# Kernel tuning notes

Measured on AMD Instinct MI355X. Metric: run time of the kernel, lower is better.

Reference implementation:

```python
import jax, jax.numpy as jnp
import numpy as np

DIM = 768
N_HEADS = 12
HEAD_DIM = DIM // N_HEADS
MLP_DIM = 3072
DEPTH = 12
B, N = 16, 512


def setup_inputs() -> dict:
    key = jax.random.key(0)
    ks = jax.random.split(key, 12)
    s = 0.02
    return {
        "x": jax.random.normal(ks[0], (B, N, DIM), dtype=jnp.float32),
        "ln_w": jnp.ones((DIM,), jnp.float32),
        "ln_b": jnp.zeros((DIM,), jnp.float32),
        "wq": jax.random.normal(ks[1], (DIM, DIM), jnp.float32) * s,
        "bq": jnp.zeros((DIM,), jnp.float32),
        "wk": jax.random.normal(ks[2], (DIM, DIM), jnp.float32) * s,
        "bk": jnp.zeros((DIM,), jnp.float32),
        "wv": jax.random.normal(ks[3], (DIM, DIM), jnp.float32) * s,
        "bv": jnp.zeros((DIM,), jnp.float32),
        "w1": jax.random.normal(ks[4], (DIM, MLP_DIM), jnp.float32) * s,
        "b1": jnp.zeros((MLP_DIM,), jnp.float32),
        "w2": jax.random.normal(ks[5], (MLP_DIM, DIM), jnp.float32) * s,
        "b2": jnp.zeros((DIM,), jnp.float32),
    }


def _layernorm(x, w, b):
    mu = jnp.mean(x, axis=-1, keepdims=True)
    var = jnp.var(x, axis=-1, keepdims=True)
    return (x - mu) * jax.lax.rsqrt(var + 1e-5) * w + b


def _mha(x, wq, bq, wk, bk, wv, bv):
    # x: [b, n, dim]; weights stored as [in, out]
    def heads(t):
        return t.reshape(B, N, N_HEADS, HEAD_DIM).transpose(0, 2, 1, 3)  # b h n d
    q = heads(x @ wq + bq)
    k = heads(x @ wk + bk)
    v = heads(x @ wv + bv)
    scores = jnp.einsum('bhqd,bhkd->bhqk', q, k) / np.sqrt(HEAD_DIM).astype(np.float32)
    attn = jax.nn.softmax(scores, axis=-1)
    o = jnp.einsum('bhqk,bhkd->bhqd', attn, v)
    return o.transpose(0, 2, 1, 3).reshape(B, N, DIM)


def reference(x, ln_w, ln_b, wq, bq, wk, bk, wv, bv, w1, b1, w2, b2):
    # Dropout is identity in eval mode. Same weights reused each depth iteration.
    for _ in range(DEPTH):
        x = _mha(_layernorm(x, ln_w, ln_b), wq, bq, wk, bk, wv, bv) + x
        h = _layernorm(x, ln_w, ln_b)
        h = jax.nn.gelu(h @ w1 + b1, approximate=False) @ w2 + b2
        x = h + x
    return x
```

## Files before the change

kernel.cpp:

```cpp
#include <hip/hip_runtime.h>

typedef __bf16 bf16x8 __attribute__((ext_vector_type(8)));
typedef float f32x4 __attribute__((ext_vector_type(4)));
typedef unsigned short ushort8_t __attribute__((ext_vector_type(8)));
typedef unsigned short ushort4_t __attribute__((ext_vector_type(4)));

#define MFMA16(a, b, c) __builtin_amdgcn_mfma_f32_16x16x32_bf16((a), (b), (c), 0, 0, 0)

#define GLOAD16(gp, lp)                                                        \
  __builtin_amdgcn_global_load_lds(                                            \
      (__attribute__((address_space(1))) void*)(gp),                           \
      (__attribute__((address_space(3))) void*)(lp), 16, 0, 0)

__device__ __forceinline__ unsigned short f2bf(float f) {
  unsigned u = __builtin_bit_cast(unsigned, f);
  return (unsigned short)((u + 0x7FFFu + ((u >> 16) & 1u)) >> 16);
}

__global__ __launch_bounds__(256) void transpose_f2b(
    const float* __restrict__ src, unsigned short* __restrict__ dst,
    int Kdim, int Ndim) {
  long i = (long)blockIdx.x * 256 + threadIdx.x;
  if (i >= (long)Kdim * Ndim) return;
  int n = (int)(i / Kdim);
  int kk = (int)(i - (long)n * Kdim);
  dst[i] = f2bf(src[(long)kk * Ndim + n]);
}

__global__ __launch_bounds__(256) void ln_kernel(
    const float* __restrict__ x, const float* __restrict__ gw,
    const float* __restrict__ gb, unsigned short* __restrict__ h) {
  const int row = blockIdx.x * 4 + (threadIdx.x >> 6);
  const int l = threadIdx.x & 63;
  const float* xr = x + (long)row * 768;
  f32x4 va[3];
#pragma unroll
  for (int i = 0; i < 3; i++) va[i] = *(const f32x4*)(xr + i * 256 + l * 4);
  float s = 0.f, ss = 0.f;
#pragma unroll
  for (int i = 0; i < 3; i++)
#pragma unroll
    for (int j = 0; j < 4; j++) {
      float t = va[i][j];
      s += t;
      ss += t * t;
    }
#pragma unroll
  for (int off = 1; off < 64; off <<= 1) {
    s += __shfl_xor(s, off, 64);
    ss += __shfl_xor(ss, off, 64);
  }
  const float mu = s * (1.f / 768.f);
  const float var = ss * (1.f / 768.f) - mu * mu;
  const float inv = rsqrtf(var + 1e-5f);
  unsigned short* hp = h + (long)row * 768;
#pragma unroll
  for (int i = 0; i < 3; i++) {
    f32x4 wv = *(const f32x4*)(gw + i * 256 + l * 4);
    f32x4 bv = *(const f32x4*)(gb + i * 256 + l * 4);
    ushort4_t o;
#pragma unroll
    for (int j = 0; j < 4; j++) o[j] = f2bf((va[i][j] - mu) * inv * wv[j] + bv[j]);
    *(ushort4_t*)(hp + i * 256 + l * 4) = o;
  }
}

__global__ __launch_bounds__(256) void transpose_v(
    const unsigned short* __restrict__ v, unsigned short* __restrict__ vt) {
  __shared__ unsigned short t[64 * 65];
  const int n0 = blockIdx.x * 64;
  const int bh = blockIdx.y;
  const int tid = threadIdx.x;
  {
    const int n = tid >> 2, d0 = (tid & 3) * 16;
    const unsigned short* s = v + ((long)bh * 512 + n0 + n) * 64 + d0;
    ushort8_t r0 = *(const ushort8_t*)s;
    ushort8_t r1 = *(const ushort8_t*)(s + 8);
#pragma unroll
    for (int j = 0; j < 8; j++) {
      t[n * 65 + d0 + j] = r0[j];
      t[n * 65 + d0 + 8 + j] = r1[j];
    }
  }
  __syncthreads();
  {
    const int d = tid >> 2, nb = (tid & 3) * 16;
    ushort8_t r0, r1;
#pragma unroll
    for (int j = 0; j < 8; j++) {
      r0[j] = t[(nb + j) * 65 + d];
      r1[j] = t[(nb + 8 + j) * 65 + d];
    }
    unsigned short* o = vt + ((long)bh * 64 + d) * 512 + n0 + nb;
    *(ushort8_t*)o = r0;
    *(ushort8_t*)(o + 8) = r1;
  }
}

enum { EPI_QKV = 0, EPI_GELU = 1, EPI_RES = 2 };

template <int EPI, int MREP>
__global__ __launch_bounds__(256) void gemm_bt(
    const unsigned short* __restrict__ A, const unsigned short* __restrict__ BT,
    int K, const float* __restrict__ bb0, const float* __restrict__ bb1,
    const float* __restrict__ bb2, unsigned short* __restrict__ o0,
    unsigned short* __restrict__ o1, unsigned short* __restrict__ o2,
    float* oF) {
  constexpr int BM = MREP * 32;
  constexpr int ABUF = BM * 32;
  __shared__ unsigned short As[2][ABUF];
  __shared__ unsigned short Bs[2][128 * 32];
  const int tid = threadIdx.x;
  const int w = tid >> 6, l = tid & 63;
  const int lr = l & 15, lg = l >> 4;
  const int wr = w >> 1, wc = w & 1;

  const int nx = gridDim.x;
  const int nwg = nx * gridDim.y;
  int wg = blockIdx.y * nx + blockIdx.x;
  {
    const int qq = nwg >> 3, rr = nwg & 7;
    const int xcd = wg & 7, idx = wg >> 3;
    wg = (xcd < rr ? xcd * (qq + 1) : rr * (qq + 1) + (xcd - rr) * qq) + idx;
  }
  const int bx = wg % nx, by = wg / nx;
  const int m0 = by * BM, n0 = bx * 128;

  const unsigned short* Ag =
      A + (long)(m0 + w * (BM / 4) + (l >> 2)) * K + (l & 3) * 8;
  const unsigned short* Bg = BT + (long)(n0 + w * 32 + (l >> 2)) * K + (l & 3) * 8;
  unsigned short* AsW = &As[0][w * (BM / 4) * 32 + l * 8];
  unsigned short* BsW = &Bs[0][w * 1024 + l * 8];

  auto stage = [&](int buf, int kt) {
    const unsigned short* ag = Ag + kt * 32;
    const unsigned short* bg = Bg + kt * 32;
    unsigned short* aw = AsW + buf * ABUF;
    unsigned short* bw = BsW + buf * 4096;
#pragma unroll
    for (int i = 0; i < BM / 64; i++) GLOAD16(ag + i * 16 * K, aw + i * 512);
    GLOAD16(bg, bw);
    GLOAD16(bg + 16 * K, bw + 512);
  };

  f32x4 acc[MREP][4] = {};
  const int nk = K >> 5;
  stage(0, 0);
  __syncthreads();
  for (int kt = 0; kt < nk; ++kt) {
    const int cur = kt & 1;
    if (kt + 1 < nk) stage(cur ^ 1, kt + 1);
    const unsigned short* Ab = &As[cur][0];
    const unsigned short* Bb = &Bs[cur][0];
    bf16x8 a[MREP], b[4];
#pragma unroll
    for (int i = 0; i < MREP; i++)
      a[i] = *(const bf16x8*)(Ab + (wr * MREP * 16 + i * 16 + lr) * 32 + lg * 8);
#pragma unroll
    for (int j = 0; j < 4; j++)
      b[j] = *(const bf16x8*)(Bb + (wc * 64 + j * 16 + lr) * 32 + lg * 8);
#pragma unroll
    for (int i = 0; i < MREP; i++)
#pragma unroll
      for (int j = 0; j < 4; j++) acc[i][j] = MFMA16(a[i], b[j], acc[i][j]);
    __syncthreads();
  }

  if (EPI == EPI_QKV) {
    const int whichq = n0 / 768;
    const int cc0 = n0 - whichq * 768;
    const float* bias = whichq == 0 ? bb0 : whichq == 1 ? bb1 : bb2;
    unsigned short* dst = whichq == 0 ? o0 : whichq == 1 ? o1 : o2;
#pragma unroll
    for (int i = 0; i < MREP; i++) {
      const int r = m0 + wr * MREP * 16 + i * 16 + lg * 4;
#pragma unroll
      for (int j = 0; j < 4; j++) {
        const int ccol = cc0 + wc * 64 + j * 16 + lr;
        const int hd = ccol >> 6, d = ccol & 63;
        const float bv = bias[ccol];
#pragma unroll
        for (int q = 0; q < 4; q++) {
          const int row = r + q;
          const int bidx = row >> 9, n = row & 511;
          const long addr = ((long)(bidx * 12 + hd) * 512 + n) * 64 + d;
          dst[addr] = f2bf(acc[i][j][q] + bv);
        }
      }
    }
  } else if (EPI == EPI_GELU) {
#pragma unroll
    for (int i = 0; i < MREP; i++) {
      const int r = m0 + wr * MREP * 16 + i * 16 + lg * 4;
#pragma unroll
      for (int j = 0; j < 4; j++) {
        const int c = n0 + wc * 64 + j * 16 + lr;
        const float bv = bb0[c];
#pragma unroll
        for (int q = 0; q < 4; q++) {
          float v = acc[i][j][q] + bv;
          const float u = v * (0.7978845608f + 0.0356774081f * v * v);
          const float g = v / (1.0f + __expf(-2.0f * u));
          o0[(long)(r + q) * 3072 + c] = f2bf(g);
        }
      }
    }
  } else {
#pragma unroll
    for (int i = 0; i < MREP; i++) {
      const int r = m0 + wr * MREP * 16 + i * 16 + lg * 4;
#pragma unroll
      for (int j = 0; j < 4; j++) {
        const int c = n0 + wc * 64 + j * 16 + lr;
        const float bv = bb0[c];
#pragma unroll
        for (int q = 0; q < 4; q++) {
          const long addr = (long)(r + q) * 768 + c;
          oF[addr] = acc[i][j][q] + bv + oF[addr];
        }
      }
    }
  }
}

__global__ __launch_bounds__(256) void attn_kernel(
    const unsigned short* __restrict__ qg, const unsigned short* __restrict__ kg,
    const unsigned short* __restrict__ vtg, float* __restrict__ x) {
  __shared__ unsigned short Qs[128 * 64];
  __shared__ unsigned short Ks[2][64 * 64];
  __shared__ unsigned short Vt[2][64 * 64];
  __shared__ unsigned short Ps[4][32 * 64];
  const int qt = blockIdx.x, h = blockIdx.y, b = blockIdx.z;
  const int bh = b * 12 + h;
  const int tid = threadIdx.x, w = tid >> 6, l = tid & 63;
  const int lr = l & 15, lg = l >> 4;

  const unsigned short* qrow =
      qg + ((long)bh * 512 + qt * 128 + w * 32 + (l >> 3)) * 64 + (l & 7) * 8;
  unsigned short* QsW = &Qs[w * 2048 + l * 8];
#pragma unroll
  for (int cc = 0; cc < 4; cc++) GLOAD16(qrow + cc * 8 * 64, QsW + cc * 512);

  const unsigned short* krow =
      kg + ((long)bh * 512 + w * 16 + (l >> 3)) * 64 + (l & 7) * 8;
  const unsigned short* vrow =
      vtg + ((long)bh * 64 + w * 16 + (l >> 3)) * 512 + (l & 7) * 8;
  unsigned short* KsW = &Ks[0][w * 1024 + l * 8];
  unsigned short* VtW = &Vt[0][w * 1024 + l * 8];
  unsigned short* Pw = &Ps[w][0];

  auto stageKV = [&](int buf, int kt) {
#pragma unroll
    for (int cc = 0; cc < 2; cc++) {
      GLOAD16(krow + (kt * 64 + cc * 8) * 64, KsW + buf * 4096 + cc * 512);
      GLOAD16(vrow + cc * 8 * 512 + kt * 64, VtW + buf * 4096 + cc * 512);
    }
  };
  stageKV(0, 0);
  __syncthreads();

  bf16x8 qa[2][2];
#pragma unroll
  for (int mi = 0; mi < 2; mi++)
#pragma unroll
    for (int ds = 0; ds < 2; ds++) {
      qa[mi][ds] =
          *(const bf16x8*)(Qs + (w * 32 + mi * 16 + lr) * 64 + ds * 32 + lg * 8);
#pragma unroll
      for (int e = 0; e < 8; e++)
        qa[mi][ds][e] = (__bf16)(0.125f * (float)qa[mi][ds][e]);
    }

  float lsum[8] = {};
  f32x4 o[2][4] = {};

  for (int kt = 0; kt < 8; ++kt) {
    const int cur = kt & 1;
    if (kt < 7) stageKV(cur ^ 1, kt + 1);

    f32x4 s[2][4] = {};
#pragma unroll
    for (int ds = 0; ds < 2; ++ds) {
      bf16x8 kb[4];
#pragma unroll
      for (int nj = 0; nj < 4; nj++)
        kb[nj] = *(const bf16x8*)(&Ks[cur][0] + (nj * 16 + lr) * 64 + ds * 32 + lg * 8);
#pragma unroll
      for (int mi = 0; mi < 2; mi++)
#pragma unroll
        for (int nj = 0; nj < 4; nj++) s[mi][nj] = MFMA16(qa[mi][ds], kb[nj], s[mi][nj]);
    }

#pragma unroll
    for (int mi = 0; mi < 2; mi++)
#pragma unroll
      for (int nj = 0; nj < 4; nj++)
#pragma unroll
        for (int q = 0; q < 4; q++) {
          const float p = __expf(s[mi][nj][q]);
          lsum[mi * 4 + q] += p;
          Pw[(mi * 16 + lg * 4 + q) * 64 + nj * 16 + lr] = f2bf(p);
        }

#pragma unroll
    for (int ks = 0; ks < 2; ++ks) {
      bf16x8 pa[2], vb[4];
#pragma unroll
      for (int mi = 0; mi < 2; mi++)
        pa[mi] = *(const bf16x8*)(Pw + (mi * 16 + lr) * 64 + ks * 32 + lg * 8);
#pragma unroll
      for (int dj = 0; dj < 4; dj++)
        vb[dj] = *(const bf16x8*)(&Vt[cur][0] + (dj * 16 + lr) * 64 + ks * 32 + lg * 8);
#pragma unroll
      for (int mi = 0; mi < 2; mi++)
#pragma unroll
        for (int dj = 0; dj < 4; dj++) o[mi][dj] = MFMA16(pa[mi], vb[dj], o[mi][dj]);
    }
    __syncthreads();
  }

#pragma unroll
  for (int i = 0; i < 8; i++) {
#pragma unroll
    for (int off = 1; off < 16; off <<= 1) lsum[i] += __shfl_xor(lsum[i], off, 64);
  }

#pragma unroll
  for (int mi = 0; mi < 2; mi++) {
#pragma unroll
    for (int q = 0; q < 4; q++) {
      const int n = qt * 128 + w * 32 + mi * 16 + lg * 4 + q;
      const float inv = 1.0f / lsum[mi * 4 + q];
      const long base = ((long)(b * 512 + n)) * 768 + h * 64;
#pragma unroll
      for (int dj = 0; dj < 4; dj++) {
        const long a = base + dj * 16 + lr;
        x[a] = x[a] + o[mi][dj][q] * inv;
      }
    }
  }
}

extern "C" void kernel_launch(void* const* d_in, const int* in_sizes, int n_in,
                              void* d_out, int out_size, void* d_ws,
                              size_t ws_size, hipStream_t stream) {
  const float* x_in = (const float*)d_in[0];
  const float* ln_w = (const float*)d_in[1];
  const float* ln_b = (const float*)d_in[2];
  const float* wq = (const float*)d_in[3];
  const float* bq = (const float*)d_in[4];
  const float* wk = (const float*)d_in[5];
  const float* bk = (const float*)d_in[6];
  const float* wv = (const float*)d_in[7];
  const float* bv = (const float*)d_in[8];
  const float* w1 = (const float*)d_in[9];
  const float* b1 = (const float*)d_in[10];
  const float* w2 = (const float*)d_in[11];
  const float* b2 = (const float*)d_in[12];

  char* p = (char*)d_ws;
  float* xw = (float*)p;            p += 8192L * 768 * 4;
  unsigned short* hbuf = (unsigned short*)p;  p += 8192L * 768 * 2;
  unsigned short* wqkvT = (unsigned short*)p; p += 2304L * 768 * 2;
  unsigned short* w1T = (unsigned short*)p;   p += 3072L * 768 * 2;
  unsigned short* w2T = (unsigned short*)p;   p += 768L * 3072 * 2;
  unsigned short* qb = (unsigned short*)p;
  unsigned short* kb = qb + 6291456L;
  unsigned short* vb = kb + 6291456L;
  unsigned short* vt = vb + 6291456L;
  unsigned short* gbuf = qb;

  hipMemcpyAsync(xw, x_in, 8192L * 768 * 4, hipMemcpyDeviceToDevice, stream);

  transpose_f2b<<<(768 * 768 + 255) / 256, 256, 0, stream>>>(wq, wqkvT, 768, 768);
  transpose_f2b<<<(768 * 768 + 255) / 256, 256, 0, stream>>>(wk, wqkvT + 589824L, 768, 768);
  transpose_f2b<<<(768 * 768 + 255) / 256, 256, 0, stream>>>(wv, wqkvT + 1179648L, 768, 768);
  transpose_f2b<<<(768 * 3072 + 255) / 256, 256, 0, stream>>>(w1, w1T, 768, 3072);
  transpose_f2b<<<(768 * 3072 + 255) / 256, 256, 0, stream>>>(w2, w2T, 3072, 768);

  for (int layer = 0; layer < 12; ++layer) {
    ln_kernel<<<2048, 256, 0, stream>>>(xw, ln_w, ln_b, hbuf);
    gemm_bt<EPI_QKV, 4><<<dim3(18, 64), 256, 0, stream>>>(
        hbuf, wqkvT, 768, bq, bk, bv, qb, kb, vb, nullptr);
    transpose_v<<<dim3(8, 192), 256, 0, stream>>>(vb, vt);
    attn_kernel<<<dim3(4, 12, 16), 256, 0, stream>>>(qb, kb, vt, xw);
    ln_kernel<<<2048, 256, 0, stream>>>(xw, ln_w, ln_b, hbuf);
    gemm_bt<EPI_GELU, 4><<<dim3(24, 64), 256, 0, stream>>>(
        hbuf, w1T, 768, b1, nullptr, nullptr, gbuf, nullptr, nullptr, nullptr);
    gemm_bt<EPI_RES, 2><<<dim3(6, 128), 256, 0, stream>>>(
        gbuf, w2T, 3072, b2, nullptr, nullptr, nullptr, nullptr, nullptr, xw);
  }

  hipMemcpyAsync(d_out, xw, 8192L * 768 * 4, hipMemcpyDeviceToDevice, stream);
}
```

Before: 2.856 ms.

## Store GEMM and attention LDS tiles in MFMA fragment order

Reorganizes the shared-memory layout of GEMM A/B tiles and attention Q/K/V/P tiles so that each 16x32 MFMA operand sub-tile is stored contiguously in the order lanes read it. Global-to-LDS loads now write lane-ordered 16-byte chunks, and fragment reads become a simple l*8 offset. The aim is to remove LDS bank conflicts on the 64-byte-stride fragment reads and simplify address arithmetic. In exchange, global loads now fetch 64-byte row segments per 16-row group, which may reduce coalescing per instruction, and the P write pattern changes.

```diff
diff --git a/kernel.cpp b/kernel.cpp
--- a/kernel.cpp
+++ b/kernel.cpp
@@ -107,9 +107,10 @@
     unsigned short* __restrict__ o1, unsigned short* __restrict__ o2,
     float* oF) {
   constexpr int BM = MREP * 32;
-  constexpr int ABUF = BM * 32;
+  constexpr int ASUB = 2 * MREP;
+  constexpr int ABUF = ASUB * 512;
   __shared__ unsigned short As[2][ABUF];
-  __shared__ unsigned short Bs[2][128 * 32];
+  __shared__ unsigned short Bs[2][8 * 512];
   const int tid = threadIdx.x;
   const int w = tid >> 6, l = tid & 63;
   const int lr = l & 15, lg = l >> 4;
@@ -126,21 +127,21 @@
   const int bx = wg % nx, by = wg / nx;
   const int m0 = by * BM, n0 = bx * 128;
 
-  const unsigned short* Ag =
-      A + (long)(m0 + w * (BM / 4) + (l >> 2)) * K + (l & 3) * 8;
-  const unsigned short* Bg = BT + (long)(n0 + w * 32 + (l >> 2)) * K + (l & 3) * 8;
-  unsigned short* AsW = &As[0][w * (BM / 4) * 32 + l * 8];
-  unsigned short* BsW = &Bs[0][w * 1024 + l * 8];
+  const unsigned short* Agl = A + (long)(m0 + lr) * K + lg * 8;
+  const unsigned short* Bgl = BT + (long)(n0 + lr) * K + lg * 8;
 
   auto stage = [&](int buf, int kt) {
-    const unsigned short* ag = Ag + kt * 32;
-    const unsigned short* bg = Bg + kt * 32;
-    unsigned short* aw = AsW + buf * ABUF;
-    unsigned short* bw = BsW + buf * 4096;
-#pragma unroll
-    for (int i = 0; i < BM / 64; i++) GLOAD16(ag + i * 16 * K, aw + i * 512);
-    GLOAD16(bg, bw);
-    GLOAD16(bg + 16 * K, bw + 512);
+    const int kk = kt * 32;
+#pragma unroll
+    for (int t = 0; t < ASUB / 4; t++) {
+      const int s = w + t * 4;
+      GLOAD16(Agl + (long)(s * 16) * K + kk, &As[buf][s * 512 + l * 8]);
+    }
+#pragma unroll
+    for (int t = 0; t < 2; t++) {
+      const int s = w + t * 4;
+      GLOAD16(Bgl + (long)(s * 16) * K + kk, &Bs[buf][s * 512 + l * 8]);
+    }
   };
 
   f32x4 acc[MREP][4] = {};
@@ -150,15 +151,13 @@
   for (int kt = 0; kt < nk; ++kt) {
     const int cur = kt & 1;
     if (kt + 1 < nk) stage(cur ^ 1, kt + 1);
-    const unsigned short* Ab = &As[cur][0];
-    const unsigned short* Bb = &Bs[cur][0];
     bf16x8 a[MREP], b[4];
 #pragma unroll
     for (int i = 0; i < MREP; i++)
-      a[i] = *(const bf16x8*)(Ab + (wr * MREP * 16 + i * 16 + lr) * 32 + lg * 8);
+      a[i] = *(const bf16x8*)(&As[cur][(wr * MREP + i) * 512 + l * 8]);
 #pragma unroll
     for (int j = 0; j < 4; j++)
-      b[j] = *(const bf16x8*)(Bb + (wc * 64 + j * 16 + lr) * 32 + lg * 8);
+      b[j] = *(const bf16x8*)(&Bs[cur][(wc * 4 + j) * 512 + l * 8]);
 #pragma unroll
     for (int i = 0; i < MREP; i++)
 #pragma unroll
@@ -226,34 +225,32 @@
 __global__ __launch_bounds__(256) void attn_kernel(
     const unsigned short* __restrict__ qg, const unsigned short* __restrict__ kg,
     const unsigned short* __restrict__ vtg, float* __restrict__ x) {
-  __shared__ unsigned short Qs[128 * 64];
-  __shared__ unsigned short Ks[2][64 * 64];
-  __shared__ unsigned short Vt[2][64 * 64];
-  __shared__ unsigned short Ps[4][32 * 64];
+  __shared__ unsigned short Qs[16 * 512];
+  __shared__ unsigned short Ks[2][8 * 512];
+  __shared__ unsigned short Vt[2][8 * 512];
+  __shared__ unsigned short Ps[4][4 * 512];
   const int qt = blockIdx.x, h = blockIdx.y, b = blockIdx.z;
   const int bh = b * 12 + h;
   const int tid = threadIdx.x, w = tid >> 6, l = tid & 63;
   const int lr = l & 15, lg = l >> 4;
 
-  const unsigned short* qrow =
-      qg + ((long)bh * 512 + qt * 128 + w * 32 + (l >> 3)) * 64 + (l & 7) * 8;
-  unsigned short* QsW = &Qs[w * 2048 + l * 8];
-#pragma unroll
-  for (int cc = 0; cc < 4; cc++) GLOAD16(qrow + cc * 8 * 64, QsW + cc * 512);
-
-  const unsigned short* krow =
-      kg + ((long)bh * 512 + w * 16 + (l >> 3)) * 64 + (l & 7) * 8;
-  const unsigned short* vrow =
-      vtg + ((long)bh * 64 + w * 16 + (l >> 3)) * 512 + (l & 7) * 8;
-  unsigned short* KsW = &Ks[0][w * 1024 + l * 8];
-  unsigned short* VtW = &Vt[0][w * 1024 + l * 8];
-  unsigned short* Pw = &Ps[w][0];
+#pragma unroll
+  for (int t = 0; t < 4; t++) {
+    const int s = w + t * 4;
+    const int rb = s >> 1, ds = s & 1;
+    GLOAD16(qg + ((long)bh * 512 + qt * 128 + rb * 16 + lr) * 64 + ds * 32 + lg * 8,
+            &Qs[s * 512 + l * 8]);
+  }
 
   auto stageKV = [&](int buf, int kt) {
 #pragma unroll
-    for (int cc = 0; cc < 2; cc++) {
-      GLOAD16(krow + (kt * 64 + cc * 8) * 64, KsW + buf * 4096 + cc * 512);
-      GLOAD16(vrow + cc * 8 * 512 + kt * 64, VtW + buf * 4096 + cc * 512);
+    for (int t = 0; t < 2; t++) {
+      const int s = w + t * 4;
+      const int rb = s >> 1, ds = s & 1;
+      GLOAD16(kg + ((long)bh * 512 + kt * 64 + rb * 16 + lr) * 64 + ds * 32 + lg * 8,
+              &Ks[buf][s * 512 + l * 8]);
+      GLOAD16(vtg + ((long)bh * 64 + rb * 16 + lr) * 512 + kt * 64 + ds * 32 + lg * 8,
+              &Vt[buf][s * 512 + l * 8]);
     }
   };
   stageKV(0, 0);
@@ -264,13 +261,13 @@
   for (int mi = 0; mi < 2; mi++)
 #pragma unroll
     for (int ds = 0; ds < 2; ds++) {
-      qa[mi][ds] =
-          *(const bf16x8*)(Qs + (w * 32 + mi * 16 + lr) * 64 + ds * 32 + lg * 8);
+      qa[mi][ds] = *(const bf16x8*)(&Qs[((w * 2 + mi) * 2 + ds) * 512 + l * 8]);
 #pragma unroll
       for (int e = 0; e < 8; e++)
         qa[mi][ds][e] = (__bf16)(0.125f * (float)qa[mi][ds][e]);
     }
 
+  unsigned short* Pw = &Ps[w][0];
   float lsum[8] = {};
   f32x4 o[2][4] = {};
 
@@ -284,7 +281,7 @@
       bf16x8 kb[4];
 #pragma unroll
       for (int nj = 0; nj < 4; nj++)
-        kb[nj] = *(const bf16x8*)(&Ks[cur][0] + (nj * 16 + lr) * 64 + ds * 32 + lg * 8);
+        kb[nj] = *(const bf16x8*)(&Ks[cur][(nj * 2 + ds) * 512 + l * 8]);
 #pragma unroll
       for (int mi = 0; mi < 2; mi++)
 #pragma unroll
@@ -294,23 +291,27 @@
 #pragma unroll
     for (int mi = 0; mi < 2; mi++)
 #pragma unroll
-      for (int nj = 0; nj < 4; nj++)
+      for (int nj = 0; nj < 4; nj++) {
+        const int sub = mi * 2 + (nj >> 1);
+        const int chunk = (nj * 2 + (lr >> 3)) & 3;
+        const int pbase = sub * 512 + chunk * 128 + lg * 32 + (lr & 7);
 #pragma unroll
         for (int q = 0; q < 4; q++) {
           const float p = __expf(s[mi][nj][q]);
           lsum[mi * 4 + q] += p;
-          Pw[(mi * 16 + lg * 4 + q) * 64 + nj * 16 + lr] = f2bf(p);
+          Pw[pbase + q * 8] = f2bf(p);
         }
+      }
 
 #pragma unroll
     for (int ks = 0; ks < 2; ++ks) {
       bf16x8 pa[2], vb[4];
 #pragma unroll
       for (int mi = 0; mi < 2; mi++)
-        pa[mi] = *(const bf16x8*)(Pw + (mi * 16 + lr) * 64 + ks * 32 + lg * 8);
+        pa[mi] = *(const bf16x8*)(Pw + (mi * 2 + ks) * 512 + l * 8);
 #pragma unroll
       for (int dj = 0; dj < 4; dj++)
-        vb[dj] = *(const bf16x8*)(&Vt[cur][0] + (dj * 16 + lr) * 64 + ks * 32 + lg * 8);
+        vb[dj] = *(const bf16x8*)(&Vt[cur][(dj * 2 + ks) * 512 + l * 8]);
 #pragma unroll
       for (int mi = 0; mi < 2; mi++)
 #pragma unroll
```

Result: slower. 3.721 ms (+30.3%).
